# Optimization experiments

Hardware: AMD Instinct MI355X
Metric: run time of the kernel (lower is better)

## Reference

```python
import jax, jax.numpy as jnp
import numpy as np

B, N, DIM = 4, 1024, 1024
H, D = 16, 64          # num_heads, head_dim
SW = 256               # sliding_window
ROPE_BASE = 10000.0
LN_EPS = 1e-5


def _layernorm(x, w, b):
    mu = jnp.mean(x, axis=-1, keepdims=True)
    var = jnp.mean((x - mu) ** 2, axis=-1, keepdims=True)
    return (x - mu) * jax.lax.rsqrt(var + LN_EPS) * w + b


def _rotate_half(x):
    x1, x2 = jnp.split(x, 2, axis=-1)
    return jnp.concatenate([-x2, x1], axis=-1)


def setup_inputs() -> dict:
    key = jax.random.key(0)
    ks = jax.random.split(key, 8)
    s = 0.02
    return {
        "x": jax.random.normal(ks[0], (B, N, DIM), dtype=jnp.float32),
        "qkv_w": jax.random.normal(ks[1], (3 * H * D, DIM), dtype=jnp.float32) * s,
        "qn_w": jnp.ones((D,), jnp.float32),
        "qn_b": jnp.zeros((D,), jnp.float32),
        "kn_w": jnp.ones((D,), jnp.float32),
        "kn_b": jnp.zeros((D,), jnp.float32),
        "sinks": jax.random.normal(ks[2], (H,), dtype=jnp.float32),
        "proj_w": jax.random.normal(ks[3], (DIM, H * D), dtype=jnp.float32) * s,
        "proj_b": jnp.zeros((DIM,), jnp.float32),
    }


def reference(x, qkv_w, qn_w, qn_b, kn_w, kn_b, sinks, proj_w, proj_b):
    Bx, Nx, _ = x.shape
    # fused QKV projection -> [3, B, H, N, D]
    qkv = (x @ qkv_w.T).reshape(Bx, Nx, 3, H, D).transpose(2, 0, 3, 1, 4)
    q, k, v = qkv[0], qkv[1], qkv[2]
    # qk-norm (LayerNorm over head_dim)
    q = _layernorm(q, qn_w, qn_b)
    k = _layernorm(k, kn_w, kn_b)
    # 1d RoPE (DeepseekV3-style: emb = cat(freqs, freqs), rotate_half)
    inv_freq = 1.0 / (ROPE_BASE ** (jnp.arange(0, D, 2, dtype=jnp.float32) / D))
    freqs = jnp.arange(Nx, dtype=jnp.float32)[:, None] * inv_freq[None, :]  # [N, D/2]
    emb = jnp.concatenate([freqs, freqs], axis=-1)                           # [N, D]
    cos, sin = jnp.cos(emb), jnp.sin(emb)
    q = q * cos + _rotate_half(q) * sin
    k = k * cos + _rotate_half(k) * sin
    # sliding-window causal mask with attention sinks
    sm_scale = 1.0 / np.sqrt(D)
    scores = jnp.einsum("bhqd,bhkd->bhqk", q, k) * sm_scale  # [B,H,N,N]
    i = jnp.arange(Nx)[:, None]
    j = jnp.arange(Nx)[None, :]
    allowed = (j <= i) & (j > i - SW)
    scores = jnp.where(allowed, scores, -jnp.inf)
    # append sink logit per head, softmax, drop sink column
    sink_col = jnp.broadcast_to(sinks[None, :, None, None], (Bx, H, Nx, 1))
    logits = jnp.concatenate([scores, sink_col], axis=-1)
    probs = jax.nn.softmax(logits, axis=-1)[..., :-1]
    out = jnp.einsum("bhqk,bhkd->bhqd", probs, v)
    out = out.transpose(0, 2, 1, 3).reshape(Bx, Nx, H * D)
    return out @ proj_w.T + proj_b
```

## Files before the change

### kernel.cpp

```cpp
#include <hip/hip_runtime.h>
#include <stdint.h>

typedef unsigned short u16;
typedef __bf16 bf16x8 __attribute__((ext_vector_type(8)));
typedef float f32x4 __attribute__((ext_vector_type(4)));

__device__ __forceinline__ float b2f(u16 u) {
  union { uint32_t i; float f; } x; x.i = ((uint32_t)u) << 16; return x.f;
}
__device__ __forceinline__ u16 f2b(float f) {
  union { float f; uint32_t i; } x; x.f = f;
  uint32_t r = x.i + 0x7fffu + ((x.i >> 16) & 1u);
  return (u16)(r >> 16);
}
__device__ __forceinline__ void gload_lds16(const u16* g, u16* l) {
  __builtin_amdgcn_global_load_lds(
      (const __attribute__((address_space(1))) void*)g,
      (__attribute__((address_space(3))) void*)l, 16, 0, 0);
}

__launch_bounds__(256)
__global__ void cvt_bf16(const float* __restrict__ x, const float* __restrict__ wq,
                         const float* __restrict__ wp, u16* __restrict__ dst) {
  const int i = (blockIdx.x * 256 + threadIdx.x) * 4;
  const float* src; int off;
  if (i < 4194304)      { src = x;  off = i; }
  else if (i < 7340032) { src = wq; off = i - 4194304; }
  else                  { src = wp; off = i - 7340032; }
  const float4 v = *(const float4*)(src + off);
  ushort4 o;
  o.x = f2b(v.x); o.y = f2b(v.y); o.z = f2b(v.z); o.w = f2b(v.w);
  *(ushort4*)(dst + i) = o;
}

__launch_bounds__(256)
__global__ void rope_tab(float* __restrict__ tab) {
  const int tid = blockIdx.x * 256 + threadIdx.x;
  const int pos = tid >> 6, d = tid & 63, i = d & 31;
  const float f = pos * exp2f(i * -0.41524101186092029f);
  float s, c;
  sincosf(f, &s, &c);
  *(float2*)(tab + tid * 2) = make_float2(c, s);
}

template<int MODE>
__launch_bounds__(256)
__global__ void gemm128(const u16* __restrict__ A, const u16* __restrict__ Bw,
                        void* __restrict__ Cp, const float* __restrict__ bias, int K) {
  __shared__ __align__(16) u16 As[128 * 32];
  __shared__ __align__(16) u16 Bs[128 * 32];
  const int t = threadIdx.x;
  const int w = t >> 6, l = t & 63, lr = l & 15, lg = l >> 4;
  const int m0 = blockIdx.y * 128, n0 = blockIdx.x * 128;
  const int wm = (w >> 1) * 64, wn = (w & 1) * 64;
  const int srow = w * 32 + (l >> 2);
  const int scol = (l & 3) * 8;
  const u16* ga0 = A  + (m0 + srow) * K + scol;
  const u16* ga1 = ga0 + 16 * K;
  const u16* gb0 = Bw + (n0 + srow) * K + scol;
  const u16* gb1 = gb0 + 16 * K;
  u16* la0 = As + w * 1024;
  u16* la1 = As + w * 1024 + 512;
  u16* lb0 = Bs + w * 1024;
  u16* lb1 = Bs + w * 1024 + 512;

  f32x4 acc[4][4] = {};
  const int nk = K >> 5;
  for (int kt = 0; kt < nk; ++kt) {
    const int ko = kt * 32;
    __syncthreads();
    gload_lds16(ga0 + ko, la0);
    gload_lds16(ga1 + ko, la1);
    gload_lds16(gb0 + ko, lb0);
    gload_lds16(gb1 + ko, lb1);
    __syncthreads();
    bf16x8 af[4], bfr[4];
#pragma unroll
    for (int i = 0; i < 4; ++i)
      af[i] = *(const bf16x8*)(As + (wm + i * 16 + lr) * 32 + lg * 8);
#pragma unroll
    for (int j = 0; j < 4; ++j)
      bfr[j] = *(const bf16x8*)(Bs + (wn + j * 16 + lr) * 32 + lg * 8);
#pragma unroll
    for (int i = 0; i < 4; ++i)
#pragma unroll
      for (int j = 0; j < 4; ++j)
        acc[i][j] = __builtin_amdgcn_mfma_f32_16x16x32_bf16(af[i], bfr[j], acc[i][j], 0, 0, 0);
  }
#pragma unroll
  for (int i = 0; i < 4; ++i)
#pragma unroll
    for (int j = 0; j < 4; ++j)
#pragma unroll
      for (int r = 0; r < 4; ++r) {
        const int gm = m0 + wm + i * 16 + lg * 4 + r;
        const int gn = n0 + wn + j * 16 + lr;
        const float v = acc[i][j][r];
        if (MODE == 0) {
          const int which = gn >> 10, hh = (gn >> 6) & 15, dd = gn & 63;
          const int bb = gm >> 10, pp = gm & 1023;
          ((u16*)Cp)[which * 4194304 + ((bb * 16 + hh) << 16) + (pp << 6) + dd] = f2b(v);
        } else {
          ((float*)Cp)[(gm << 10) + gn] = v + bias[gn];
        }
      }
}

__launch_bounds__(256)
__global__ void ln_rope(u16* __restrict__ qk, const float* __restrict__ qn_w,
                        const float* __restrict__ qn_b, const float* __restrict__ kn_w,
                        const float* __restrict__ kn_b, const float* __restrict__ tab) {
  const int t = threadIdx.x;
  const int wid = blockIdx.x * 4 + (t >> 6);
  const int l = t & 63;
  const int row = wid * 2 + (l >> 5);
  const int j = l & 31, d0 = j * 2;
  const int which = row >> 16;
  const int pos = row & 1023;
  const float* wgt = which ? kn_w : qn_w;
  const float* bia = which ? kn_b : qn_b;
  u16* p = qk + row * 64 + d0;
  const ushort2 raw = *(const ushort2*)p;
  float v0 = b2f(raw.x), v1 = b2f(raw.y);
  float s = v0 + v1;
#pragma unroll
  for (int off = 1; off < 32; off <<= 1) s += __shfl_xor(s, off);
  const float mu = s * 0.015625f;
  const float e0 = v0 - mu, e1 = v1 - mu;
  float qsum = e0 * e0 + e1 * e1;
#pragma unroll
  for (int off = 1; off < 32; off <<= 1) qsum += __shfl_xor(qsum, off);
  const float rstd = rsqrtf(qsum * 0.015625f + 1e-5f);
  const float n0 = e0 * rstd * wgt[d0] + bia[d0];
  const float n1 = e1 * rstd * wgt[d0 + 1] + bia[d0 + 1];
  const float p0 = __shfl_xor(n0, 16);
  const float p1 = __shfl_xor(n1, 16);
  const bool lo = (d0 < 32);
  const float r0 = lo ? -p0 : p0, r1 = lo ? -p1 : p1;
  const float4 cs = *(const float4*)(tab + (pos * 64 + d0) * 2);
  ushort2 o;
  o.x = f2b(n0 * cs.x + r0 * cs.y);
  o.y = f2b(n1 * cs.z + r1 * cs.w);
  *(ushort2*)p = o;
}

__launch_bounds__(256)
__global__ void vtrans(const u16* __restrict__ v, u16* __restrict__ vt) {
  __shared__ u16 tile[128 * 65];
  const int t = threadIdx.x;
  const int bh = blockIdx.x >> 3;
  const int n0 = (blockIdx.x & 7) * 128;
  const u16* src = v + bh * 65536 + n0 * 64;
#pragma unroll
  for (int it = 0; it < 8; ++it) {
    const int e = (it * 256 + t) * 4;
    const int n = e >> 6, d = e & 63;
    const ushort4 x = *(const ushort4*)(src + n * 64 + d);
    tile[n * 65 + d + 0] = x.x;
    tile[n * 65 + d + 1] = x.y;
    tile[n * 65 + d + 2] = x.z;
    tile[n * 65 + d + 3] = x.w;
  }
  __syncthreads();
  u16* dst = vt + bh * 65536 + n0;
#pragma unroll
  for (int it = 0; it < 8; ++it) {
    const int o = (it * 256 + t) * 4;
    const int d = o >> 7, c = o & 127;
    ushort4 y;
    y.x = tile[(c + 0) * 65 + d];
    y.y = tile[(c + 1) * 65 + d];
    y.z = tile[(c + 2) * 65 + d];
    y.w = tile[(c + 3) * 65 + d];
    *(ushort4*)(dst + d * 1024 + c) = y;
  }
}

__launch_bounds__(256)
__global__ void attn_kernel(const u16* __restrict__ q, const u16* __restrict__ k,
                            const u16* __restrict__ vt, const float* __restrict__ sinks,
                            u16* __restrict__ ao) {
  __shared__ __align__(16) u16 pbuf[4][16 * 296];
  const int t = threadIdx.x, w = t >> 6, l = t & 63, lr = l & 15, lg = l >> 4;
  const int bid = blockIdx.x;
  const int qb = bid & 15, h = (bid >> 4) & 15, b = bid >> 8;
  const int i0 = qb * 64 + w * 16;
  const int bh = b * 16 + h;
  const u16* qp = q + bh * 65536;
  const u16* kp = k + bh * 65536;
  const u16* vp = vt + bh * 65536;
  u16* pb = pbuf[w];

  const bf16x8 qf0 = *(const bf16x8*)(qp + (i0 + lr) * 64 + lg * 8);
  const bf16x8 qf1 = *(const bf16x8*)(qp + (i0 + lr) * 64 + 32 + lg * 8);
  const int ja = i0 - 256;

  f32x4 sacc[17];
#pragma unroll
  for (int jt = 0; jt < 17; ++jt) {
    const int jr = ja + jt * 16 + lr;
    const int jc = jr < 0 ? 0 : jr;
    const bf16x8 kf0 = *(const bf16x8*)(kp + jc * 64 + lg * 8);
    const bf16x8 kf1 = *(const bf16x8*)(kp + jc * 64 + 32 + lg * 8);
    f32x4 a = {0.f, 0.f, 0.f, 0.f};
    a = __builtin_amdgcn_mfma_f32_16x16x32_bf16(qf0, kf0, a, 0, 0, 0);
    a = __builtin_amdgcn_mfma_f32_16x16x32_bf16(qf1, kf1, a, 0, 0, 0);
    sacc[jt] = a;
  }
  const float sink = sinks[h];
  float mx[4] = {-1e30f, -1e30f, -1e30f, -1e30f};
#pragma unroll
  for (int jt = 0; jt < 17; ++jt)
#pragma unroll
    for (int r = 0; r < 4; ++r) {
      const int qi = i0 + lg * 4 + r;
      const int jg = ja + jt * 16 + lr;
      const bool ok = (jg >= 0) && (jg <= qi) && (jg > qi - 256);
      const float sv = ok ? sacc[jt][r] * 0.125f : -1e30f;
      sacc[jt][r] = sv;
      mx[r] = fmaxf(mx[r], sv);
    }
#pragma unroll
  for (int off = 1; off < 16; off <<= 1)
#pragma unroll
    for (int r = 0; r < 4; ++r) mx[r] = fmaxf(mx[r], __shfl_xor(mx[r], off));
#pragma unroll
  for (int r = 0; r < 4; ++r) mx[r] = fmaxf(mx[r], sink);
  float sum[4] = {0.f, 0.f, 0.f, 0.f};
#pragma unroll
  for (int jt = 0; jt < 17; ++jt)
#pragma unroll
    for (int r = 0; r < 4; ++r) {
      const float e = __expf(sacc[jt][r] - mx[r]);
      sacc[jt][r] = e;
      sum[r] += e;
    }
#pragma unroll
  for (int off = 1; off < 16; off <<= 1)
#pragma unroll
    for (int r = 0; r < 4; ++r) sum[r] += __shfl_xor(sum[r], off);
  float inv[4];
#pragma unroll
  for (int r = 0; r < 4; ++r) inv[r] = 1.0f / (sum[r] + __expf(sink - mx[r]));
  {
    ushort4 z; z.x = 0; z.y = 0; z.z = 0; z.w = 0;
    *(ushort4*)(pb + (l >> 2) * 296 + 272 + (l & 3) * 4) = z;
  }
#pragma unroll
  for (int jt = 0; jt < 17; ++jt)
#pragma unroll
    for (int r = 0; r < 4; ++r)
      pb[(lg * 4 + r) * 296 + jt * 16 + lr] = f2b(sacc[jt][r] * inv[r]);

  f32x4 oacc[4] = {};
#pragma unroll
  for (int ks = 0; ks < 9; ++ks) {
    const bf16x8 pf = *(const bf16x8*)(pb + lr * 296 + ks * 32 + lg * 8);
#pragma unroll
    for (int dt = 0; dt < 4; ++dt) {
      int jg = ja + ks * 32 + lg * 8;
      jg = jg < 0 ? 0 : (jg > 1016 ? 1016 : jg);
      const bf16x8 vf = *(const bf16x8*)(vp + (dt * 16 + lr) * 1024 + jg);
      oacc[dt] = __builtin_amdgcn_mfma_f32_16x16x32_bf16(pf, vf, oacc[dt], 0, 0, 0);
    }
  }
#pragma unroll
  for (int dt = 0; dt < 4; ++dt)
#pragma unroll
    for (int r = 0; r < 4; ++r) {
      const int m = (b << 10) + i0 + lg * 4 + r;
      ao[(m << 10) + (h << 6) + dt * 16 + lr] = f2b(oacc[dt][r]);
    }
}

extern "C" void kernel_launch(void* const* d_in, const int* in_sizes, int n_in,
                              void* d_out, int out_size, void* d_ws, size_t ws_size,
                              hipStream_t stream) {
  const float* x      = (const float*)d_in[0];
  const float* qkv_w  = (const float*)d_in[1];
  const float* qn_w   = (const float*)d_in[2];
  const float* qn_b   = (const float*)d_in[3];
  const float* kn_w   = (const float*)d_in[4];
  const float* kn_b   = (const float*)d_in[5];
  const float* sinks  = (const float*)d_in[6];
  const float* proj_w = (const float*)d_in[7];
  const float* proj_b = (const float*)d_in[8];
  float* out = (float*)d_out;
  u16* ws     = (u16*)d_ws;
  u16* qkv    = ws;
  u16* xb     = ws + 12582912;
  u16* wqkvb  = ws + 16777216;
  u16* wprojb = ws + 19922944;
  float* tab  = (float*)(ws + 20971520);
  u16* ao     = ws + 21233664;
  u16* vtw    = ws + 12582912;

  cvt_bf16<<<8192, 256, 0, stream>>>(x, qkv_w, proj_w, xb);
  rope_tab<<<256, 256, 0, stream>>>(tab);
  gemm128<0><<<dim3(24, 32), 256, 0, stream>>>(xb, wqkvb, qkv, nullptr, 1024);
  ln_rope<<<16384, 256, 0, stream>>>(qkv, qn_w, qn_b, kn_w, kn_b, tab);
  vtrans<<<512, 256, 0, stream>>>(qkv + 8388608, vtw);
  attn_kernel<<<1024, 256, 0, stream>>>(qkv, qkv + 4194304, vtw, sinks, ao);
  gemm128<1><<<dim3(8, 32), 256, 0, stream>>>(ao, wprojb, out, proj_b, 1024);
}
```

Baseline: 218.8 us.

## Stage K and V tiles in LDS with XOR swizzle for attention

The attention kernel now cooperatively loads the block's K window (320 rows) and the transposed V window into shared memory via global_load_lds, so all four waves share one copy instead of each wave reading K/V from global memory. To make this conflict-free, ln_rope writes K rows with an XOR-swizzled column order and vtrans writes V^T in 64-key blocks with a swizzled slot layout. ln_rope is also vectorized to process 8 elements per lane with fewer shuffles, and the P buffer reuses the K LDS region after a barrier. Shared memory use rises to about 80KB per block, which may limit occupancy, and the extra barriers add some sync cost.

Measured after the change: 199.3 us. 8.9% less time.

```diff
diff --git a/kernel.cpp b/kernel.cpp
--- a/kernel.cpp
+++ b/kernel.cpp
@@ -110,38 +110,60 @@
 __global__ void ln_rope(u16* __restrict__ qk, const float* __restrict__ qn_w,
                         const float* __restrict__ qn_b, const float* __restrict__ kn_w,
                         const float* __restrict__ kn_b, const float* __restrict__ tab) {
-  const int t = threadIdx.x;
-  const int wid = blockIdx.x * 4 + (t >> 6);
-  const int l = t & 63;
-  const int row = wid * 2 + (l >> 5);
-  const int j = l & 31, d0 = j * 2;
+  const int t = threadIdx.x, l = t & 63;
+  const int wv = blockIdx.x * 4 + (t >> 6);
+  const int row = wv * 8 + (l >> 3);
+  const int c = l & 7;
   const int which = row >> 16;
   const int pos = row & 1023;
   const float* wgt = which ? kn_w : qn_w;
   const float* bia = which ? kn_b : qn_b;
-  u16* p = qk + row * 64 + d0;
-  const ushort2 raw = *(const ushort2*)p;
-  float v0 = b2f(raw.x), v1 = b2f(raw.y);
-  float s = v0 + v1;
-#pragma unroll
-  for (int off = 1; off < 32; off <<= 1) s += __shfl_xor(s, off);
+  const u16* src = qk + row * 64 + c * 8;
+  const ushort4 ra = *(const ushort4*)(src);
+  const ushort4 rb = *(const ushort4*)(src + 4);
+  float v[8] = {b2f(ra.x), b2f(ra.y), b2f(ra.z), b2f(ra.w),
+                b2f(rb.x), b2f(rb.y), b2f(rb.z), b2f(rb.w)};
+  float s = 0.f;
+#pragma unroll
+  for (int i = 0; i < 8; ++i) s += v[i];
+#pragma unroll
+  for (int off = 1; off < 8; off <<= 1) s += __shfl_xor(s, off);
   const float mu = s * 0.015625f;
-  const float e0 = v0 - mu, e1 = v1 - mu;
-  float qsum = e0 * e0 + e1 * e1;
-#pragma unroll
-  for (int off = 1; off < 32; off <<= 1) qsum += __shfl_xor(qsum, off);
-  const float rstd = rsqrtf(qsum * 0.015625f + 1e-5f);
-  const float n0 = e0 * rstd * wgt[d0] + bia[d0];
-  const float n1 = e1 * rstd * wgt[d0 + 1] + bia[d0 + 1];
-  const float p0 = __shfl_xor(n0, 16);
-  const float p1 = __shfl_xor(n1, 16);
-  const bool lo = (d0 < 32);
-  const float r0 = lo ? -p0 : p0, r1 = lo ? -p1 : p1;
-  const float4 cs = *(const float4*)(tab + (pos * 64 + d0) * 2);
-  ushort2 o;
-  o.x = f2b(n0 * cs.x + r0 * cs.y);
-  o.y = f2b(n1 * cs.z + r1 * cs.w);
-  *(ushort2*)p = o;
+  float e[8], qs = 0.f;
+#pragma unroll
+  for (int i = 0; i < 8; ++i) { e[i] = v[i] - mu; qs += e[i] * e[i]; }
+#pragma unroll
+  for (int off = 1; off < 8; off <<= 1) qs += __shfl_xor(qs, off);
+  const float rstd = rsqrtf(qs * 0.015625f + 1e-5f);
+  const int d0 = c * 8;
+  float wb[8], bb[8];
+  *(float4*)(wb) = *(const float4*)(wgt + d0);
+  *(float4*)(wb + 4) = *(const float4*)(wgt + d0 + 4);
+  *(float4*)(bb) = *(const float4*)(bia + d0);
+  *(float4*)(bb + 4) = *(const float4*)(bia + d0 + 4);
+  float n[8], r[8];
+#pragma unroll
+  for (int i = 0; i < 8; ++i) n[i] = e[i] * rstd * wb[i] + bb[i];
+#pragma unroll
+  for (int i = 0; i < 8; ++i) r[i] = __shfl_xor(n[i], 4);
+  const bool lo = (c < 4);
+#pragma unroll
+  for (int i = 0; i < 8; ++i) r[i] = lo ? -r[i] : r[i];
+  float cs[16];
+  *(float4*)(cs)      = *(const float4*)(tab + (pos * 64 + d0) * 2);
+  *(float4*)(cs + 4)  = *(const float4*)(tab + (pos * 64 + d0) * 2 + 4);
+  *(float4*)(cs + 8)  = *(const float4*)(tab + (pos * 64 + d0) * 2 + 8);
+  *(float4*)(cs + 12) = *(const float4*)(tab + (pos * 64 + d0) * 2 + 12);
+  ushort4 oa, ob;
+  float o[8];
+#pragma unroll
+  for (int i = 0; i < 8; ++i) o[i] = n[i] * cs[2 * i] + r[i] * cs[2 * i + 1];
+  oa.x = f2b(o[0]); oa.y = f2b(o[1]); oa.z = f2b(o[2]); oa.w = f2b(o[3]);
+  ob.x = f2b(o[4]); ob.y = f2b(o[5]); ob.z = f2b(o[6]); ob.w = f2b(o[7]);
+  const int dstc = which ? (c ^ (pos & 7)) : c;
+  u16* dst = qk + row * 64 + dstc * 8;
+  *(ushort4*)(dst) = oa;
+  *(ushort4*)(dst + 4) = ob;
 }
 
 __launch_bounds__(256)
@@ -162,7 +184,7 @@
     tile[n * 65 + d + 3] = x.w;
   }
   __syncthreads();
-  u16* dst = vt + bh * 65536 + n0;
+  u16* dst = vt + bh * 65536;
 #pragma unroll
   for (int it = 0; it < 8; ++it) {
     const int o = (it * 256 + t) * 4;
@@ -172,15 +194,19 @@
     y.y = tile[(c + 1) * 65 + d];
     y.z = tile[(c + 2) * 65 + d];
     y.w = tile[(c + 3) * 65 + d];
-    *(ushort4*)(dst + d * 1024 + c) = y;
-  }
-}
-
-__launch_bounds__(256)
+    const int gj = n0 + c;
+    const int nb = gj >> 6, jl = gj & 63;
+    const int slot = (jl >> 3) ^ (d & 7);
+    *(ushort4*)(dst + nb * 4096 + d * 64 + slot * 8 + (jl & 7)) = y;
+  }
+}
+
+__launch_bounds__(256, 2)
 __global__ void attn_kernel(const u16* __restrict__ q, const u16* __restrict__ k,
                             const u16* __restrict__ vt, const float* __restrict__ sinks,
                             u16* __restrict__ ao) {
-  __shared__ __align__(16) u16 pbuf[4][16 * 296];
+  __shared__ __align__(16) u16 Ks[20480];
+  __shared__ __align__(16) u16 Vs[20480];
   const int t = threadIdx.x, w = t >> 6, l = t & 63, lr = l & 15, lg = l >> 4;
   const int bid = blockIdx.x;
   const int qb = bid & 15, h = (bid >> 4) & 15, b = bid >> 8;
@@ -189,25 +215,41 @@
   const u16* qp = q + bh * 65536;
   const u16* kp = k + bh * 65536;
   const u16* vp = vt + bh * 65536;
-  u16* pb = pbuf[w];
-
+  const int j0 = qb * 64 - 256;
+
+#pragma unroll
+  for (int i = 0; i < 10; ++i) {
+    const int c = w * 10 + i;
+    int off = j0 * 64 + c * 512 + l * 8;
+    off = off < 0 ? 0 : off;
+    gload_lds16(kp + off, Ks + c * 512);
+  }
+#pragma unroll
+  for (int i = 0; i < 10; ++i) {
+    const int c = w * 10 + i;
+    const int n = c >> 3, p = c & 7;
+    int nb = qb - 4 + n;
+    nb = nb < 0 ? 0 : nb;
+    gload_lds16(vp + nb * 4096 + p * 512 + l * 8, Vs + c * 512);
+  }
   const bf16x8 qf0 = *(const bf16x8*)(qp + (i0 + lr) * 64 + lg * 8);
   const bf16x8 qf1 = *(const bf16x8*)(qp + (i0 + lr) * 64 + 32 + lg * 8);
-  const int ja = i0 - 256;
-
+  __syncthreads();
+
+  const int key = lr & 7;
   f32x4 sacc[17];
 #pragma unroll
   for (int jt = 0; jt < 17; ++jt) {
-    const int jr = ja + jt * 16 + lr;
-    const int jc = jr < 0 ? 0 : jr;
-    const bf16x8 kf0 = *(const bf16x8*)(kp + jc * 64 + lg * 8);
-    const bf16x8 kf1 = *(const bf16x8*)(kp + jc * 64 + 32 + lg * 8);
+    const int r = w * 16 + jt * 16 + lr;
+    const bf16x8 kf0 = *(const bf16x8*)(Ks + r * 64 + ((lg ^ key)) * 8);
+    const bf16x8 kf1 = *(const bf16x8*)(Ks + r * 64 + (((lg + 4) ^ key)) * 8);
     f32x4 a = {0.f, 0.f, 0.f, 0.f};
     a = __builtin_amdgcn_mfma_f32_16x16x32_bf16(qf0, kf0, a, 0, 0, 0);
     a = __builtin_amdgcn_mfma_f32_16x16x32_bf16(qf1, kf1, a, 0, 0, 0);
     sacc[jt] = a;
   }
   const float sink = sinks[h];
+  const int ja = i0 - 256;
   float mx[4] = {-1e30f, -1e30f, -1e30f, -1e30f};
 #pragma unroll
   for (int jt = 0; jt < 17; ++jt)
@@ -242,6 +284,9 @@
   float inv[4];
 #pragma unroll
   for (int r = 0; r < 4; ++r) inv[r] = 1.0f / (sum[r] + __expf(sink - mx[r]));
+
+  __syncthreads();
+  u16* pb = Ks + w * 4736;
   {
     ushort4 z; z.x = 0; z.y = 0; z.z = 0; z.w = 0;
     *(ushort4*)(pb + (l >> 2) * 296 + 272 + (l & 3) * 4) = z;
@@ -258,9 +303,11 @@
     const bf16x8 pf = *(const bf16x8*)(pb + lr * 296 + ks * 32 + lg * 8);
 #pragma unroll
     for (int dt = 0; dt < 4; ++dt) {
-      int jg = ja + ks * 32 + lg * 8;
-      jg = jg < 0 ? 0 : (jg > 1016 ? 1016 : jg);
-      const bf16x8 vf = *(const bf16x8*)(vp + (dt * 16 + lr) * 1024 + jg);
+      int r = w * 16 + ks * 32 + lg * 8;
+      r = r < 320 ? r : 0;
+      const int n = r >> 6, jl = r & 63;
+      const int slot = (jl >> 3) ^ (lr & 7);
+      const bf16x8 vf = *(const bf16x8*)(Vs + n * 4096 + (dt * 16 + lr) * 64 + slot * 8);
       oacc[dt] = __builtin_amdgcn_mfma_f32_16x16x32_bf16(pf, vf, oacc[dt], 0, 0, 0);
     }
   }
@@ -298,7 +345,7 @@
   cvt_bf16<<<8192, 256, 0, stream>>>(x, qkv_w, proj_w, xb);
   rope_tab<<<256, 256, 0, stream>>>(tab);
   gemm128<0><<<dim3(24, 32), 256, 0, stream>>>(xb, wqkvb, qkv, nullptr, 1024);
-  ln_rope<<<16384, 256, 0, stream>>>(qkv, qn_w, qn_b, kn_w, kn_b, tab);
+  ln_rope<<<4096, 256, 0, stream>>>(qkv, qn_w, qn_b, kn_w, kn_b, tab);
   vtrans<<<512, 256, 0, stream>>>(qkv + 8388608, vtw);
   attn_kernel<<<1024, 256, 0, stream>>>(qkv, qkv + 4194304, vtw, sinks, ao);
   gemm128<1><<<dim3(8, 32), 256, 0, stream>>>(ao, wprojb, out, proj_b, 1024);
```
